# Kernel tuning notes

Measured on AMD Instinct MI355X. Metric: run time of the kernel, lower is better.

Reference implementation:

```python
import jax, jax.numpy as jnp
import numpy as np

# Config mirrors CrossAttentionAudio2T(dim=768, n_head=12, num_frames=16, spec_frames=8,
# attn_all_frame=True, audio_patch=196, time_encoding=False, use_stpos=True)
B, T, N, NA, ST, D, H = 4, 8, 196, 196, 8, 768, 12
HD = D // H
SCALE = HD ** -0.5


def setup_inputs() -> dict:
    key = jax.random.key(0)
    ks = jax.random.split(key, 12)
    r = lambda k, s: jax.random.normal(k, s, dtype=jnp.float32)
    return dict(
        t_x=r(ks[0], (B, T * N, D)),
        audio=r(ks[1], (NA + 2, B * ST, D)),
        vmae_space_pos=SCALE * r(ks[2], (N, D)),
        audio_space_pos=SCALE * r(ks[3], (NA, D)),
        vmae_temporal_pos=SCALE * r(ks[4], (T, D)),
        audio_temporal_pos=SCALE * r(ks[5], (ST, D)),
        q_w=0.02 * r(ks[6], (D, D)),
        q_b=jnp.zeros((D,), jnp.float32),
        kv_w=0.02 * r(ks[7], (2 * D, D)),
        kv_b=jnp.zeros((2 * D,), jnp.float32),
        proj_w=0.02 * r(ks[8], (D, D)),
        proj_b=jnp.zeros((D,), jnp.float32),
    )


def reference(t_x, audio, vmae_space_pos, audio_space_pos, vmae_temporal_pos,
              audio_temporal_pos, q_w, q_b, kv_w, kv_b, proj_w, proj_b):
    # --- video query tokens: add spatial + temporal pos embeds ---
    x = t_x.reshape(B, T, N, D) + vmae_space_pos          # [B,T,N,D] + [N,D]
    x = x.transpose(0, 2, 1, 3) + vmae_temporal_pos       # [B,N,T,D] + [T,D]
    x = x.transpose(0, 2, 1, 3).reshape(B, T * N, D)      # 'b n t d -> b (t n) d'

    # --- audio key/value tokens: drop 2 lead tokens, add pos embeds ---
    a = audio[2:].reshape(NA, B, ST, D).transpose(1, 2, 0, 3)  # 'n (b t) d -> b t n d'
    a = a + audio_space_pos                                    # [B,ST,NA,D] + [NA,D]
    a = a.transpose(0, 2, 1, 3) + audio_temporal_pos           # [B,NA,ST,D] + [ST,D]
    a = a.reshape(B, NA * ST, D)                               # 'b n t d -> b (n t) d'

    # --- projections ---
    q = (x @ q_w.T + q_b).reshape(B, T * N, H, HD).transpose(0, 2, 1, 3)   # [B,H,Lq,HD]
    kv = (a @ kv_w.T + kv_b).reshape(B, NA * ST, 2, H, HD)
    k = kv[:, :, 0].transpose(0, 2, 1, 3)                                  # [B,H,Lk,HD]
    v = kv[:, :, 1].transpose(0, 2, 1, 3)

    # --- scaled dot-product cross-attention (full score matrix, as in source) ---
    attn = jax.nn.softmax(jnp.einsum('bhqd,bhkd->bhqk', q * SCALE, k), axis=-1)
    o = jnp.einsum('bhqk,bhkd->bhqd', attn, v)
    o = o.transpose(0, 2, 1, 3).reshape(B, T * N, D)
    return o @ proj_w.T + proj_b
```

## Files before the change

### kernel.cpp

```cpp
#include <hip/hip_runtime.h>

typedef short s8v __attribute__((ext_vector_type(8)));
typedef short s4v __attribute__((ext_vector_type(4)));
typedef float f4v __attribute__((ext_vector_type(4)));

#define LQ 1568
#define LK 1568
#define NH 12

__device__ __forceinline__ unsigned short f2bf(float f) {
  union { float f; unsigned u; } x; x.f = f;
  unsigned r = x.u + 0x7FFFu + ((x.u >> 16) & 1u);
  return (unsigned short)(r >> 16);
}

__global__ void prep_xa(const float* __restrict__ t_x, const float* __restrict__ audio,
                        const float* __restrict__ sp, const float* __restrict__ asp,
                        const float* __restrict__ tp, const float* __restrict__ atp,
                        unsigned short* __restrict__ xb, unsigned short* __restrict__ ab,
                        int total4) {
  int i = blockIdx.x * 256 + threadIdx.x;
  if (i >= 2 * total4) return;
  if (i < total4) {
    int d4 = (i % 192) * 4;
    int row = i / 192;
    int l = row % LQ;
    int t = l / 196, n = l % 196;
    float4 a  = *(const float4*)(t_x + (size_t)i * 4);
    float4 s  = *(const float4*)(sp + n * 768 + d4);
    float4 tt = *(const float4*)(tp + t * 768 + d4);
    ushort4 o;
    o.x = f2bf(a.x + s.x + tt.x);
    o.y = f2bf(a.y + s.y + tt.y);
    o.z = f2bf(a.z + s.z + tt.z);
    o.w = f2bf(a.w + s.w + tt.w);
    *(ushort4*)(xb + (size_t)i * 4) = o;
  } else {
    i -= total4;
    int d4 = (i % 192) * 4;
    int row = i / 192;
    int b = row / LK;
    int r2 = row % LK;
    int na = r2 >> 3, ta = r2 & 7;
    const float* src = audio + ((size_t)(2 + na) * 32 + b * 8 + ta) * 768 + d4;
    float4 a  = *(const float4*)src;
    float4 s  = *(const float4*)(asp + na * 768 + d4);
    float4 tt = *(const float4*)(atp + ta * 768 + d4);
    ushort4 o;
    o.x = f2bf(a.x + s.x + tt.x);
    o.y = f2bf(a.y + s.y + tt.y);
    o.z = f2bf(a.z + s.z + tt.z);
    o.w = f2bf(a.w + s.w + tt.w);
    *(ushort4*)(ab + (size_t)i * 4) = o;
  }
}

__global__ void conv_w(const float* __restrict__ q_w, const float* __restrict__ kv_w,
                       const float* __restrict__ proj_w, unsigned short* __restrict__ wq,
                       unsigned short* __restrict__ wkv, unsigned short* __restrict__ wp) {
  const int n1 = 768 * 768 / 4, n2 = 1536 * 768 / 4;
  int i = blockIdx.x * 256 + threadIdx.x;
  const float* src; unsigned short* dst; int j = i;
  if (i < n1)               { src = q_w;    dst = wq;  }
  else if (i < n1 + n2)     { src = kv_w;   dst = wkv; j = i - n1; }
  else if (i < 2 * n1 + n2) { src = proj_w; dst = wp;  j = i - n1 - n2; }
  else return;
  float4 v = *(const float4*)(src + (size_t)j * 4);
  ushort4 o;
  o.x = f2bf(v.x); o.y = f2bf(v.y); o.z = f2bf(v.z); o.w = f2bf(v.w);
  *(ushort4*)(dst + (size_t)j * 4) = o;
}

__device__ __forceinline__ void gemm_mainloop(
    const unsigned short* __restrict__ A, const unsigned short* __restrict__ W,
    int K, int row0, int col0,
    unsigned short* As, unsigned short* Bs, f4v acc[4][4]) {
  const int tid = threadIdx.x;
  const int lane = tid & 63, wave = tid >> 6;
  const int wm = wave & 1, wn = wave >> 1;
  const int l15 = lane & 15, quad = lane >> 4;
  const int lr = tid >> 3, lc = (tid & 7) * 8;

  for (int k0 = 0; k0 < K; k0 += 64) {
    __syncthreads();
#pragma unroll
    for (int it = 0; it < 4; ++it) {
      int row = lr + it * 32;
      __builtin_amdgcn_global_load_lds(
          (const __attribute__((address_space(1))) unsigned int*)(A + (size_t)(row0 + row) * K + k0 + lc),
          (__attribute__((address_space(3))) unsigned int*)(As + row * 64 + lc), 16, 0, 0);
      __builtin_amdgcn_global_load_lds(
          (const __attribute__((address_space(1))) unsigned int*)(W + (size_t)(col0 + row) * K + k0 + lc),
          (__attribute__((address_space(3))) unsigned int*)(Bs + row * 64 + lc), 16, 0, 0);
    }
    __syncthreads();
#pragma unroll
    for (int kk = 0; kk < 2; ++kk) {
      s8v af[4], bf[4];
#pragma unroll
      for (int i = 0; i < 4; ++i) {
        af[i] = *(const s8v*)(As + (wm * 64 + i * 16 + l15) * 64 + kk * 32 + quad * 8);
        bf[i] = *(const s8v*)(Bs + (wn * 64 + i * 16 + l15) * 64 + kk * 32 + quad * 8);
      }
#pragma unroll
      for (int mi = 0; mi < 4; ++mi)
#pragma unroll
        for (int ni = 0; ni < 4; ++ni)
          acc[mi][ni] = __builtin_amdgcn_mfma_f32_16x16x32_bf16(af[mi], bf[ni],
                                                               acc[mi][ni], 0, 0, 0);
    }
  }
}

__global__ __launch_bounds__(256, 2) void gemm_qkv(
    const unsigned short* __restrict__ xb, const unsigned short* __restrict__ ab,
    const unsigned short* __restrict__ wq, const unsigned short* __restrict__ wkv,
    const float* __restrict__ q_b, const float* __restrict__ kv_b,
    unsigned short* __restrict__ Qs, unsigned short* __restrict__ Kb,
    unsigned short* __restrict__ Vb) {
  __shared__ __align__(16) unsigned short As[128 * 64];
  __shared__ __align__(16) unsigned short Bs[128 * 64];
  const int tid = threadIdx.x;
  const int lane = tid & 63, wave = tid >> 6;
  const int wm = wave & 1, wn = wave >> 1;
  const int l15 = lane & 15, quad = lane >> 4;
  const int row0 = blockIdx.x * 128;
  const int y = blockIdx.y;
  const bool isQ = (y < 6);
  const int col0 = (isQ ? y : y - 6) * 128;
  const unsigned short* A = isQ ? xb : ab;
  const unsigned short* W = isQ ? wq : wkv;
  const float* bias = isQ ? q_b : kv_b;

  f4v acc[4][4] = {};
  gemm_mainloop(A, W, 768, row0, col0, As, Bs, acc);

#pragma unroll
  for (int mi = 0; mi < 4; ++mi) {
    int rowg = row0 + wm * 64 + mi * 16 + quad * 4;
#pragma unroll
    for (int ni = 0; ni < 4; ++ni) {
      int colg = col0 + wn * 64 + ni * 16 + l15;
      float bv = bias[colg];
      if (!isQ && colg >= 768) {
        int oo = colg - 768;
        int h = oo >> 6, hd = oo & 63;
        int b = rowg / LK, l0 = rowg - b * LK;
        ushort4 pk;
        pk.x = f2bf(acc[mi][ni][0] + bv);
        pk.y = f2bf(acc[mi][ni][1] + bv);
        pk.z = f2bf(acc[mi][ni][2] + bv);
        pk.w = f2bf(acc[mi][ni][3] + bv);
        *(ushort4*)(Vb + ((((size_t)b * NH + h) * 392 + (l0 >> 2)) * 64 + hd) * 4) = pk;
        continue;
      }
#pragma unroll
      for (int r = 0; r < 4; ++r) {
        float v = acc[mi][ni][r] + bv;
        int row = rowg + r;
        int b = row / LQ, l = row - b * LQ;
        int h = colg >> 6, hd = colg & 63;
        if (isQ) {
          v *= 0.18033688011112042f;
          Qs[(((size_t)b * NH + h) * LQ + l) * 64 + hd] = f2bf(v);
        } else {
          Kb[(((size_t)b * NH + h) * LK + l) * 64 + hd] = f2bf(v);
        }
      }
    }
  }
}

__global__ __launch_bounds__(256, 2) void gemm_proj(
    const unsigned short* __restrict__ A, const unsigned short* __restrict__ W,
    const float* __restrict__ bias, float* __restrict__ out) {
  __shared__ __align__(16) unsigned short As[128 * 64];
  __shared__ __align__(16) unsigned short Bs[128 * 64];
  const int tid = threadIdx.x;
  const int lane = tid & 63, wave = tid >> 6;
  const int wm = wave & 1, wn = wave >> 1;
  const int l15 = lane & 15, quad = lane >> 4;
  const int row0 = blockIdx.x * 128;
  const int col0 = blockIdx.y * 128;

  f4v acc[4][4] = {};
  gemm_mainloop(A, W, 768, row0, col0, As, Bs, acc);

#pragma unroll
  for (int mi = 0; mi < 4; ++mi) {
    int rowg = row0 + wm * 64 + mi * 16 + quad * 4;
#pragma unroll
    for (int ni = 0; ni < 4; ++ni) {
      int colg = col0 + wn * 64 + ni * 16 + l15;
      float bv = bias[colg];
#pragma unroll
      for (int r = 0; r < 4; ++r)
        out[(size_t)(rowg + r) * 768 + colg] = acc[mi][ni][r] + bv;
    }
  }
}

__global__ __launch_bounds__(256, 3) void attn(
    const unsigned short* __restrict__ Q, const unsigned short* __restrict__ Kg,
    const unsigned short* __restrict__ Vsw, unsigned short* __restrict__ O) {
  __shared__ __align__(16) unsigned short Kl[112 * 72];
  __shared__ __align__(16) unsigned short Vl[112 * 64];
  const int tid = threadIdx.x;
  const int lane = tid & 63, wave = tid >> 6;
  const int l15 = lane & 15, quad = lane >> 4;
  const int bh = blockIdx.y;
  const int q0 = blockIdx.x * 128;
  const size_t base = (size_t)bh * LK * 64;

  s8v qf[2][2];
#pragma unroll
  for (int mt = 0; mt < 2; ++mt)
#pragma unroll
    for (int kk = 0; kk < 2; ++kk) {
      int row = q0 + wave * 32 + mt * 16 + l15;
      if (row > LQ - 1) row = LQ - 1;
      qf[mt][kk] = *(const s8v*)(Q + base + (size_t)row * 64 + kk * 32 + quad * 8);
    }

  f4v of[2][4] = {};
  float lr[2] = {0.0f, 0.0f};

  for (int k0 = 0; k0 < LK; k0 += 112) {
    __syncthreads();
    for (int c = tid; c < 896; c += 256) {
      int r = c >> 3, kc = c & 7;
      *(uint4*)(Kl + r * 72 + kc * 8) =
          *(const uint4*)(Kg + base + (size_t)(k0 + r) * 64 + kc * 8);
    }
    {
      const uint4* src = (const uint4*)(Vsw + base + (size_t)k0 * 64);
      uint4* dst = (uint4*)Vl;
      for (int c = tid; c < 896; c += 256) dst[c] = src[c];
    }
    __syncthreads();

#pragma unroll
    for (int nt = 0; nt < 7; ++nt) {
      s8v kf0 = *(const s8v*)(Kl + (nt * 16 + l15) * 72 + quad * 8);
      s8v kf1 = *(const s8v*)(Kl + (nt * 16 + l15) * 72 + 32 + quad * 8);
      s4v pf[2];
#pragma unroll
      for (int mt = 0; mt < 2; ++mt) {
        f4v s = {};
        s = __builtin_amdgcn_mfma_f32_16x16x32_bf16(kf0, qf[mt][0], s, 0, 0, 0);
        s = __builtin_amdgcn_mfma_f32_16x16x32_bf16(kf1, qf[mt][1], s, 0, 0, 0);
        float p0 = __builtin_amdgcn_exp2f(s[0]);
        float p1 = __builtin_amdgcn_exp2f(s[1]);
        float p2 = __builtin_amdgcn_exp2f(s[2]);
        float p3 = __builtin_amdgcn_exp2f(s[3]);
        lr[mt] += (p0 + p1) + (p2 + p3);
        union { float f; unsigned u; } a0, a1, a2, a3;
        a0.f = p0; a1.f = p1; a2.f = p2; a3.f = p3;
        union { uint2 u; s4v s; } pk;
        pk.u.x = __builtin_amdgcn_perm(a1.u, a0.u, 0x07060302u);
        pk.u.y = __builtin_amdgcn_perm(a3.u, a2.u, 0x07060302u);
        pf[mt] = pk.s;
      }
#pragma unroll
      for (int nd = 0; nd < 4; ++nd) {
        s4v vf = *(const s4v*)(Vl + ((nt * 4 + quad) << 8) + ((nd * 16 + l15) << 2));
        of[0][nd] = __builtin_amdgcn_mfma_f32_16x16x16bf16_1k(pf[0], vf, of[0][nd], 0, 0, 0);
        of[1][nd] = __builtin_amdgcn_mfma_f32_16x16x16bf16_1k(pf[1], vf, of[1][nd], 0, 0, 0);
      }
    }
  }

#pragma unroll
  for (int mt = 0; mt < 2; ++mt) {
    lr[mt] += __shfl_xor(lr[mt], 16);
    lr[mt] += __shfl_xor(lr[mt], 32);
  }

  const int b = bh / NH, h = bh - b * NH;
#pragma unroll
  for (int mt = 0; mt < 2; ++mt)
#pragma unroll
    for (int r = 0; r < 4; ++r) {
      int row = q0 + wave * 32 + mt * 16 + quad * 4 + r;
      if (row >= LQ) continue;
      float inv = 1.0f / __shfl(lr[mt], quad * 4 + r);
#pragma unroll
      for (int nd = 0; nd < 4; ++nd) {
        float v = of[mt][nd][r] * inv;
        O[((size_t)(b * LQ) + row) * 768 + h * 64 + nd * 16 + l15] = f2bf(v);
      }
    }
}

extern "C" void kernel_launch(void* const* d_in, const int* in_sizes, int n_in,
                              void* d_out, int out_size, void* d_ws, size_t ws_size,
                              hipStream_t stream) {
  const float* t_x    = (const float*)d_in[0];
  const float* audio  = (const float*)d_in[1];
  const float* sp     = (const float*)d_in[2];
  const float* asp    = (const float*)d_in[3];
  const float* tp     = (const float*)d_in[4];
  const float* atp    = (const float*)d_in[5];
  const float* q_w    = (const float*)d_in[6];
  const float* q_b    = (const float*)d_in[7];
  const float* kv_w   = (const float*)d_in[8];
  const float* kv_b   = (const float*)d_in[9];
  const float* proj_w = (const float*)d_in[10];
  const float* proj_b = (const float*)d_in[11];
  float* out = (float*)d_out;

  char* ws = (char*)d_ws;
  size_t off = 0;
  auto alloc = [&](size_t bytes) -> void* {
    void* p = ws + off;
    off += (bytes + 255) & ~(size_t)255;
    return p;
  };
  const size_t TOK = 6272;
  unsigned short* xb  = (unsigned short*)alloc(TOK * 768 * 2);
  unsigned short* ab  = (unsigned short*)alloc(TOK * 768 * 2);
  unsigned short* wq  = (unsigned short*)alloc(768 * 768 * 2);
  unsigned short* wkv = (unsigned short*)alloc(1536 * 768 * 2);
  unsigned short* wp  = (unsigned short*)alloc(768 * 768 * 2);
  unsigned short* Qs  = (unsigned short*)alloc(TOK * 768 * 2);
  unsigned short* Kb  = (unsigned short*)alloc(TOK * 768 * 2);
  unsigned short* Vb  = (unsigned short*)alloc(TOK * 768 * 2);

  dim3 blk(256);
  const int n1 = 768 * 768 / 4, n2 = 1536 * 768 / 4;
  conv_w<<<dim3((2 * n1 + n2 + 255) / 256), blk, 0, stream>>>(q_w, kv_w, proj_w, wq, wkv, wp);

  int total4 = (int)(TOK * 192);
  prep_xa<<<dim3((2 * total4 + 255) / 256), blk, 0, stream>>>(t_x, audio, sp, asp, tp, atp,
                                                              xb, ab, total4);

  gemm_qkv<<<dim3(49, 18), blk, 0, stream>>>(xb, ab, wq, wkv, q_b, kv_b, Qs, Kb, Vb);

  attn<<<dim3(13, 48), blk, 0, stream>>>(Qs, Kb, Vb, xb );

  gemm_proj<<<dim3(49, 6), blk, 0, stream>>>(xb, wp, proj_b, out);
}
```

Baseline: 245.4 us.

## Split attention over two key halves with merge kernel, fuse prep kernels

```diff
diff --git a/kernel.cpp b/kernel.cpp
--- a/kernel.cpp
+++ b/kernel.cpp
@@ -7,19 +7,41 @@
 #define LQ 1568
 #define LK 1568
 #define NH 12
+#define LQP 1664
 
 __device__ __forceinline__ unsigned short f2bf(float f) {
   union { float f; unsigned u; } x; x.f = f;
   unsigned r = x.u + 0x7FFFu + ((x.u >> 16) & 1u);
   return (unsigned short)(r >> 16);
 }
-
-__global__ void prep_xa(const float* __restrict__ t_x, const float* __restrict__ audio,
-                        const float* __restrict__ sp, const float* __restrict__ asp,
-                        const float* __restrict__ tp, const float* __restrict__ atp,
-                        unsigned short* __restrict__ xb, unsigned short* __restrict__ ab,
-                        int total4) {
+__device__ __forceinline__ float bf2f(unsigned short s) {
+  union { unsigned u; float f; } x; x.u = ((unsigned)s) << 16;
+  return x.f;
+}
+
+__global__ void prep_all(const float* __restrict__ t_x, const float* __restrict__ audio,
+                         const float* __restrict__ sp, const float* __restrict__ asp,
+                         const float* __restrict__ tp, const float* __restrict__ atp,
+                         const float* __restrict__ q_w, const float* __restrict__ kv_w,
+                         const float* __restrict__ proj_w,
+                         unsigned short* __restrict__ xb, unsigned short* __restrict__ ab,
+                         unsigned short* __restrict__ wq, unsigned short* __restrict__ wkv,
+                         unsigned short* __restrict__ wp, int total4) {
+  const int n1 = 768 * 768 / 4, n2 = 1536 * 768 / 4;
+  const int nconv = 2 * n1 + n2;
   int i = blockIdx.x * 256 + threadIdx.x;
+  if (i < nconv) {
+    const float* src; unsigned short* dst; int j = i;
+    if (i < n1)           { src = q_w;    dst = wq;  }
+    else if (i < n1 + n2) { src = kv_w;   dst = wkv; j = i - n1; }
+    else                  { src = proj_w; dst = wp;  j = i - n1 - n2; }
+    float4 v = *(const float4*)(src + (size_t)j * 4);
+    ushort4 o;
+    o.x = f2bf(v.x); o.y = f2bf(v.y); o.z = f2bf(v.z); o.w = f2bf(v.w);
+    *(ushort4*)(dst + (size_t)j * 4) = o;
+    return;
+  }
+  i -= nconv;
   if (i >= 2 * total4) return;
   if (i < total4) {
     int d4 = (i % 192) * 4;
@@ -55,22 +77,6 @@
   }
 }
 
-__global__ void conv_w(const float* __restrict__ q_w, const float* __restrict__ kv_w,
-                       const float* __restrict__ proj_w, unsigned short* __restrict__ wq,
-                       unsigned short* __restrict__ wkv, unsigned short* __restrict__ wp) {
-  const int n1 = 768 * 768 / 4, n2 = 1536 * 768 / 4;
-  int i = blockIdx.x * 256 + threadIdx.x;
-  const float* src; unsigned short* dst; int j = i;
-  if (i < n1)               { src = q_w;    dst = wq;  }
-  else if (i < n1 + n2)     { src = kv_w;   dst = wkv; j = i - n1; }
-  else if (i < 2 * n1 + n2) { src = proj_w; dst = wp;  j = i - n1 - n2; }
-  else return;
-  float4 v = *(const float4*)(src + (size_t)j * 4);
-  ushort4 o;
-  o.x = f2bf(v.x); o.y = f2bf(v.y); o.z = f2bf(v.z); o.w = f2bf(v.w);
-  *(ushort4*)(dst + (size_t)j * 4) = o;
-}
-
 __device__ __forceinline__ void gemm_mainloop(
     const unsigned short* __restrict__ A, const unsigned short* __restrict__ W,
     int K, int row0, int col0,
@@ -112,7 +118,7 @@
   }
 }
 
-__global__ __launch_bounds__(256, 2) void gemm_qkv(
+__global__ __launch_bounds__(256, 3) void gemm_qkv(
     const unsigned short* __restrict__ xb, const unsigned short* __restrict__ ab,
     const unsigned short* __restrict__ wq, const unsigned short* __restrict__ wkv,
     const float* __restrict__ q_b, const float* __restrict__ kv_b,
@@ -171,7 +177,7 @@
   }
 }
 
-__global__ __launch_bounds__(256, 2) void gemm_proj(
+__global__ __launch_bounds__(256, 3) void gemm_proj(
     const unsigned short* __restrict__ A, const unsigned short* __restrict__ W,
     const float* __restrict__ bias, float* __restrict__ out) {
   __shared__ __align__(16) unsigned short As[128 * 64];
@@ -200,9 +206,10 @@
   }
 }
 
-__global__ __launch_bounds__(256, 3) void attn(
+__global__ __launch_bounds__(256, 4) void attn(
     const unsigned short* __restrict__ Q, const unsigned short* __restrict__ Kg,
-    const unsigned short* __restrict__ Vsw, unsigned short* __restrict__ O) {
+    const unsigned short* __restrict__ Vsw,
+    unsigned short* __restrict__ Op, float* __restrict__ Lp) {
   __shared__ __align__(16) unsigned short Kl[112 * 72];
   __shared__ __align__(16) unsigned short Vl[112 * 64];
   const int tid = threadIdx.x;
@@ -210,6 +217,8 @@
   const int l15 = lane & 15, quad = lane >> 4;
   const int bh = blockIdx.y;
   const int q0 = blockIdx.x * 128;
+  const int half = blockIdx.z;
+  const int kbeg = half * 784;
   const size_t base = (size_t)bh * LK * 64;
 
   s8v qf[2][2];
@@ -225,18 +234,18 @@
   f4v of[2][4] = {};
   float lr[2] = {0.0f, 0.0f};
 
-  for (int k0 = 0; k0 < LK; k0 += 112) {
+  for (int kt = 0; kt < 7; ++kt) {
+    int k0 = kbeg + kt * 112;
     __syncthreads();
     for (int c = tid; c < 896; c += 256) {
       int r = c >> 3, kc = c & 7;
       *(uint4*)(Kl + r * 72 + kc * 8) =
           *(const uint4*)(Kg + base + (size_t)(k0 + r) * 64 + kc * 8);
     }
-    {
-      const uint4* src = (const uint4*)(Vsw + base + (size_t)k0 * 64);
-      uint4* dst = (uint4*)Vl;
-      for (int c = tid; c < 896; c += 256) dst[c] = src[c];
-    }
+    for (int c = tid; c < 896; c += 256)
+      __builtin_amdgcn_global_load_lds(
+          (const __attribute__((address_space(1))) unsigned int*)(Vsw + base + (size_t)k0 * 64 + c * 8),
+          (__attribute__((address_space(3))) unsigned int*)(Vl + c * 8), 16, 0, 0);
     __syncthreads();
 
 #pragma unroll
@@ -276,20 +285,48 @@
     lr[mt] += __shfl_xor(lr[mt], 32);
   }
 
-  const int b = bh / NH, h = bh - b * NH;
-#pragma unroll
-  for (int mt = 0; mt < 2; ++mt)
+  const size_t obase = ((size_t)(half * 48 + bh) * LQP + q0);
+#pragma unroll
+  for (int mt = 0; mt < 2; ++mt) {
 #pragma unroll
     for (int r = 0; r < 4; ++r) {
-      int row = q0 + wave * 32 + mt * 16 + quad * 4 + r;
-      if (row >= LQ) continue;
-      float inv = 1.0f / __shfl(lr[mt], quad * 4 + r);
-#pragma unroll
-      for (int nd = 0; nd < 4; ++nd) {
-        float v = of[mt][nd][r] * inv;
-        O[((size_t)(b * LQ) + row) * 768 + h * 64 + nd * 16 + l15] = f2bf(v);
-      }
-    }
+      int rowl = wave * 32 + mt * 16 + quad * 4 + r;
+#pragma unroll
+      for (int nd = 0; nd < 4; ++nd)
+        Op[(obase + rowl) * 64 + nd * 16 + l15] = f2bf(of[mt][nd][r]);
+    }
+    if (quad == 0)
+      Lp[obase + wave * 32 + mt * 16 + l15] = lr[mt];
+  }
+}
+
+__global__ void attn_merge(const unsigned short* __restrict__ Op,
+                           const float* __restrict__ Lp,
+                           unsigned short* __restrict__ Om) {
+  int i = blockIdx.x * 256 + threadIdx.x;
+  if (i >= 48 * LQ * 8) return;
+  int hd8 = (i & 7) * 8;
+  int t = i >> 3;
+  int row = t % LQ;
+  int bh = t / LQ;
+  int b = bh / NH, h = bh - b * NH;
+  const unsigned short* p0 = Op + ((size_t)bh * LQP + row) * 64 + hd8;
+  const unsigned short* p1 = Op + ((size_t)(48 + bh) * LQP + row) * 64 + hd8;
+  float inv = 1.0f / (Lp[(size_t)bh * LQP + row] + Lp[(size_t)(48 + bh) * LQP + row]);
+  ushort4 a0 = *(const ushort4*)p0, a1 = *(const ushort4*)(p0 + 4);
+  ushort4 b0 = *(const ushort4*)p1, b1 = *(const ushort4*)(p1 + 4);
+  ushort4 o0, o1;
+  o0.x = f2bf((bf2f(a0.x) + bf2f(b0.x)) * inv);
+  o0.y = f2bf((bf2f(a0.y) + bf2f(b0.y)) * inv);
+  o0.z = f2bf((bf2f(a0.z) + bf2f(b0.z)) * inv);
+  o0.w = f2bf((bf2f(a0.w) + bf2f(b0.w)) * inv);
+  o1.x = f2bf((bf2f(a1.x) + bf2f(b1.x)) * inv);
+  o1.y = f2bf((bf2f(a1.y) + bf2f(b1.y)) * inv);
+  o1.z = f2bf((bf2f(a1.z) + bf2f(b1.z)) * inv);
+  o1.w = f2bf((bf2f(a1.w) + bf2f(b1.w)) * inv);
+  unsigned short* dst = Om + ((size_t)(b * LQ) + row) * 768 + h * 64 + hd8;
+  *(ushort4*)dst = o0;
+  *(ushort4*)(dst + 4) = o1;
 }
 
 extern "C" void kernel_launch(void* const* d_in, const int* in_sizes, int n_in,
@@ -326,17 +363,22 @@
   unsigned short* Kb  = (unsigned short*)alloc(TOK * 768 * 2);
   unsigned short* Vb  = (unsigned short*)alloc(TOK * 768 * 2);
 
+  unsigned short* Op = (unsigned short*)ws;
+  float*          Lp = (float*)(ws + (size_t)2 * 48 * LQP * 64 * 2);
+  unsigned short* Om = Qs;
+
   dim3 blk(256);
   const int n1 = 768 * 768 / 4, n2 = 1536 * 768 / 4;
-  conv_w<<<dim3((2 * n1 + n2 + 255) / 256), blk, 0, stream>>>(q_w, kv_w, proj_w, wq, wkv, wp);
-
   int total4 = (int)(TOK * 192);
-  prep_xa<<<dim3((2 * total4 + 255) / 256), blk, 0, stream>>>(t_x, audio, sp, asp, tp, atp,
-                                                              xb, ab, total4);
+  int nprep = 2 * n1 + n2 + 2 * total4;
+  prep_all<<<dim3((nprep + 255) / 256), blk, 0, stream>>>(
+      t_x, audio, sp, asp, tp, atp, q_w, kv_w, proj_w, xb, ab, wq, wkv, wp, total4);
 
   gemm_qkv<<<dim3(49, 18), blk, 0, stream>>>(xb, ab, wq, wkv, q_b, kv_b, Qs, Kb, Vb);
 
-  attn<<<dim3(13, 48), blk, 0, stream>>>(Qs, Kb, Vb, xb );
-
-  gemm_proj<<<dim3(49, 6), blk, 0, stream>>>(xb, wp, proj_b, out);
-}
+  attn<<<dim3(13, 48, 2), blk, 0, stream>>>(Qs, Kb, Vb, Op, Lp);
+
+  attn_merge<<<dim3((48 * LQ * 8 + 255) / 256), blk, 0, stream>>>(Op, Lp, Om);
+
+  gemm_proj<<<dim3(49, 6), blk, 0, stream>>>(Om, wp, proj_b, out);
+}
```

Result: no change. 240.9 us (-1.8%).
